# Kernel tuning notes

Hardware: AMD Instinct MI355X
Metric: run time of the kernel (lower is better)

## Reference

```python
import jax, jax.numpy as jnp
import numpy as np

B, P, K, H, W = 32, 8, 17, 192, 192
ALPHA = 0.5
TEMP = 2.0
SIGMA = 3.0


def _bce_with_logits_mean(x, t):
    # numerically stable BCEWithLogitsLoss, reduction='mean'
    return jnp.mean(jnp.maximum(x, 0.0) - x * t + jnp.log1p(jnp.exp(-jnp.abs(x))))


def _kl_batchmean(s_logprob, t_prob):
    # torch KLDivLoss(reduction='batchmean'): sum(t * (log t - log s)) / batch
    return jnp.sum(t_prob * (jnp.log(t_prob) - s_logprob)) / s_logprob.shape[0]


def _keypoints_loss(pred, kps, vis):
    # pred: [B,K,H,W]; kps: [B,P,K,2] normalized; vis: [B,P,K] int
    b, k, h, w = pred.shape
    x = jnp.floor(kps[..., 0] * (w - 1))  # [B,P,K]; coords>=0 so floor == int()
    y = jnp.floor(kps[..., 1] * (h - 1))
    valid = ((vis > 0) & (x >= 0) & (x < w) & (y >= 0) & (y < h)).astype(pred.dtype)
    inv2s2 = 1.0 / (2.0 * SIGMA * SIGMA)
    ax = jnp.arange(w, dtype=pred.dtype)
    ay = jnp.arange(h, dtype=pred.dtype)
    # separable Gaussian: exp(-((a-x)^2+(b-y)^2)/2s^2) = gx(a)*gy(b)
    gx = jnp.exp(-(ax - x[..., None]) ** 2 * inv2s2) * valid[..., None]  # [B,P,K,W]
    gy = jnp.exp(-(ay - y[..., None]) ** 2 * inv2s2)                     # [B,P,K,H]
    # original indexes target[k][a,b] with a over grid_x (W axis); H==W required
    target = jnp.einsum('bpkw,bpkh->bkwh', gx, gy)  # [B,K,W,H] == [B,K,H,W]
    per = jnp.sum((pred - target) ** 2, axis=(1, 2, 3))          # F.mse_loss sum
    denom = jnp.sum(vis, axis=(1, 2)).astype(pred.dtype) + 1e-6
    return jnp.mean(per / denom)


def setup_inputs() -> dict:
    key = jax.random.key(0)
    k1, k2, k3, k4, k5, k6, k7 = jax.random.split(key, 7)
    return {
        's_seg_logits': jax.random.normal(k1, (B, 1, H, W), dtype=jnp.float32),
        's_pose_logits': jax.random.normal(k2, (B, K, H, W), dtype=jnp.float32),
        't_seg_logits': jax.random.normal(k3, (B, 1, H, W), dtype=jnp.float32),
        't_pose_logits': jax.random.normal(k4, (B, K, H, W), dtype=jnp.float32),
        'mask': jax.random.uniform(k5, (B, H, W), dtype=jnp.float32),
        'keypoints': jax.random.uniform(k6, (B, P, K, 2), dtype=jnp.float32),
        'visibilities': jax.random.randint(k7, (B, P, K), 0, 2, dtype=jnp.int32),
    }


def reference(s_seg_logits, s_pose_logits, t_seg_logits, t_pose_logits, mask, keypoints, visibilities):
    # task losses
    task_seg = _bce_with_logits_mean(s_seg_logits, mask[:, None])  # unsqueeze(1)
    task_pose = _keypoints_loss(s_pose_logits, keypoints, visibilities)
    task_loss = task_seg + task_pose
    # segmentation distillation (softmax over channel dim)
    s_seg_lp = jax.nn.log_softmax(s_seg_logits / TEMP, axis=1)
    t_seg_p = jax.nn.softmax(t_seg_logits / TEMP, axis=1)
    seg_distill = _kl_batchmean(s_seg_lp, t_seg_p) * TEMP ** 2
    # pose distillation (softmax over flattened K*H*W)
    s_pose_lp = jax.nn.log_softmax(s_pose_logits.reshape(s_pose_logits.shape[0], -1) / TEMP, axis=1)
    t_pose_p = jax.nn.softmax(t_pose_logits.reshape(t_pose_logits.shape[0], -1) / TEMP, axis=1)
    pose_distill = _kl_batchmean(s_pose_lp, t_pose_p) * TEMP ** 2
    distill_loss = seg_distill + pose_distill
    total = ALPHA * distill_loss + (1.0 - ALPHA) * task_loss
    return total
```

## Files before the change

### kernel.cpp

```cpp
#include <hip/hip_runtime.h>
#include <hip/hip_bf16.h>
#include <math.h>

#define B_   32
#define P_   8
#define K_   17
#define H_   192
#define W_   192
#define HW_  (H_*W_)
#define NROW (K_*HW_)
#define NROW4 (NROW/4)
#define KL_BLK_PER_ROW 153
#define KL_NBLK (B_*KL_BLK_PER_ROW)
#define BCE_NBLK 288
#define KP_SEG 3
#define KP_NBLK (B_*K_*KP_SEG)

__device__ inline float wave_red_sum(float v) {
    for (int o = 32; o; o >>= 1) v += __shfl_xor(v, o, 64);
    return v;
}
__device__ inline float wave_red_max(float v) {
    for (int o = 32; o; o >>= 1) v = fmaxf(v, __shfl_xor(v, o, 64));
    return v;
}
__device__ inline float block_sum(float v, float* sm) {
    v = wave_red_sum(v);
    int w = threadIdx.x >> 6;
    if ((threadIdx.x & 63) == 0) sm[w] = v;
    __syncthreads();
    float r = sm[0] + sm[1] + sm[2] + sm[3];
    __syncthreads();
    return r;
}
__device__ inline float block_max(float v, float* sm) {
    v = wave_red_max(v);
    int w = threadIdx.x >> 6;
    if ((threadIdx.x & 63) == 0) sm[w] = v;
    __syncthreads();
    float r = fmaxf(fmaxf(sm[0], sm[1]), fmaxf(sm[2], sm[3]));
    __syncthreads();
    return r;
}

__global__ void __launch_bounds__(256) bce_kernel(
        const float* __restrict__ x, const float* __restrict__ m,
        float* __restrict__ ws) {
    __shared__ float sm[4];
    const float4* x4 = (const float4*)x;
    const float4* m4 = (const float4*)m;
    int tid = threadIdx.x;
    size_t base = (size_t)blockIdx.x * 1024 + tid;
    float acc = 0.f;
#pragma unroll
    for (int j = 0; j < 4; j++) {
        float4 xv = x4[base + j*256];
        float4 tv = m4[base + j*256];
        acc += fmaxf(xv.x, 0.f) - xv.x*tv.x + log1pf(__expf(-fabsf(xv.x)));
        acc += fmaxf(xv.y, 0.f) - xv.y*tv.y + log1pf(__expf(-fabsf(xv.y)));
        acc += fmaxf(xv.z, 0.f) - xv.z*tv.z + log1pf(__expf(-fabsf(xv.z)));
        acc += fmaxf(xv.w, 0.f) - xv.w*tv.w + log1pf(__expf(-fabsf(xv.w)));
    }
    acc = block_sum(acc, sm);
    if (tid == 0) ws[blockIdx.x] = acc;
}

__global__ void __launch_bounds__(256) kl_kernel(
        const float* __restrict__ s, const float* __restrict__ t,
        float* __restrict__ ws) {
    __shared__ float sm[4];
    int blk = blockIdx.x;
    int b = blk / KL_BLK_PER_ROW;
    int r = blk - b*KL_BLK_PER_ROW;
    size_t base4 = (size_t)b * NROW4 + (size_t)r * 1024;
    const float4* s4 = (const float4*)s + base4;
    const float4* t4 = (const float4*)t + base4;
    int tid = threadIdx.x;

    float u[16], v[16];
#pragma unroll
    for (int j = 0; j < 4; j++) {
        float4 sv = s4[j*256 + tid];
        float4 tv = t4[j*256 + tid];
        v[j*4+0] = sv.x*0.5f; v[j*4+1] = sv.y*0.5f; v[j*4+2] = sv.z*0.5f; v[j*4+3] = sv.w*0.5f;
        u[j*4+0] = tv.x*0.5f; u[j*4+1] = tv.y*0.5f; u[j*4+2] = tv.z*0.5f; u[j*4+3] = tv.w*0.5f;
    }
    float mu = -INFINITY, mv = -INFINITY;
#pragma unroll
    for (int i = 0; i < 16; i++) { mu = fmaxf(mu, u[i]); mv = fmaxf(mv, v[i]); }
    mu = block_max(mu, sm);
    mv = block_max(mv, sm);

    float Zu = 0.f, Zv = 0.f, A = 0.f;
#pragma unroll
    for (int i = 0; i < 16; i++) {
        float e = __expf(u[i] - mu);
        Zu += e;
        A  += e * (u[i] - v[i]);
        Zv += __expf(v[i] - mv);
    }
    Zu = block_sum(Zu, sm);
    Zv = block_sum(Zv, sm);
    A  = block_sum(A,  sm);
    if (tid == 0) {
        float* o = ws + (size_t)blk * 5;
        o[0] = mu; o[1] = Zu; o[2] = mv; o[3] = Zv; o[4] = A;
    }
}

__global__ void __launch_bounds__(256) kp_kernel(
        const float* __restrict__ pred, const float* __restrict__ kps,
        const int* __restrict__ vis, float* __restrict__ ws) {
    __shared__ __align__(16) float gxs[P_][W_];
    __shared__ __align__(16) float gys[P_][H_];
    __shared__ float xk[P_], yk[P_], vld[P_];
    __shared__ float smr[4];

    int blk = blockIdx.x;
    int b   = blk / (K_*KP_SEG);
    int r   = blk - b*(K_*KP_SEG);
    int k   = r / KP_SEG;
    int seg = r - k*KP_SEG;
    int tid = threadIdx.x;

    if (tid < P_) {
        int p = tid;
        float kx = kps[((b*P_ + p)*K_ + k)*2 + 0];
        float ky = kps[((b*P_ + p)*K_ + k)*2 + 1];
        int vv   = vis[(b*P_ + p)*K_ + k];
        float fx = floorf(kx * (float)(W_ - 1));
        float fy = floorf(ky * (float)(H_ - 1));
        bool ok = (vv > 0) && (fx >= 0.f) && (fx < (float)W_) && (fy >= 0.f) && (fy < (float)H_);
        xk[p] = fx; yk[p] = fy; vld[p] = ok ? 1.0f : 0.0f;
    }
    __syncthreads();

    const float inv2s2 = 1.0f / 18.0f;
    for (int e = tid; e < P_*W_; e += 256) {
        int p = e / W_;
        int i = e - p*W_;
        float dx = (float)i - xk[p];
        float dy = (float)i - yk[p];
        gxs[p][i] = __expf(-dx*dx*inv2s2) * vld[p];
        gys[p][i] = __expf(-dy*dy*inv2s2);
    }
    __syncthreads();

    const float* pbase = pred + (size_t)(b*K_ + k) * HW_;
    float acc = 0.f;
#pragma unroll
    for (int it = 0; it < 3; it++) {
        int tau = it*256 + tid;
        int rg = tau / 48;
        int cg = tau - rg*48;
        int i0 = seg*64 + rg*4;
        int j0 = cg*4;
        float4 gx[P_], gy[P_];
#pragma unroll
        for (int p = 0; p < P_; p++) {
            gx[p] = *(const float4*)&gxs[p][i0];
            gy[p] = *(const float4*)&gys[p][j0];
        }
#pragma unroll
        for (int rr = 0; rr < 4; rr++) {
            float4 pv = *(const float4*)(pbase + (i0 + rr)*W_ + j0);
            float t0 = 0.f, t1 = 0.f, t2 = 0.f, t3 = 0.f;
#pragma unroll
            for (int p = 0; p < P_; p++) {
                float g = (rr == 0) ? gx[p].x : (rr == 1) ? gx[p].y : (rr == 2) ? gx[p].z : gx[p].w;
                t0 += g * gy[p].x;
                t1 += g * gy[p].y;
                t2 += g * gy[p].z;
                t3 += g * gy[p].w;
            }
            float d0 = pv.x - t0, d1 = pv.y - t1, d2 = pv.z - t2, d3 = pv.w - t3;
            acc += d0*d0 + d1*d1 + d2*d2 + d3*d3;
        }
    }
    acc = block_sum(acc, smr);
    if (tid == 0) ws[blk] = acc;
}

__global__ void __launch_bounds__(64) finalize_kernel(
        const float* __restrict__ ws_bce, const float* __restrict__ ws_kl,
        const float* __restrict__ ws_kp,  const int* __restrict__ vis,
        float* __restrict__ out) {
    __shared__ float skl[B_], skp[B_];
    int tid = threadIdx.x;

    float bsum = 0.f;
    for (int i = tid; i < BCE_NBLK; i += 64) bsum += ws_bce[i];
    bsum = wave_red_sum(bsum);

    if (tid < B_) {
        int b = tid;
        float Mu = -INFINITY, Zu = 0.f, Mv = -INFINITY, Zv = 0.f, A = 0.f;
        for (int j = 0; j < KL_BLK_PER_ROW; j++) {
            const float* p = ws_kl + (size_t)(b*KL_BLK_PER_ROW + j) * 5;
            float mu = p[0], zu = p[1], mv = p[2], zv = p[3], a = p[4];
            float nm = fmaxf(Mu, mu);
            float e0 = __expf(Mu - nm), e1 = __expf(mu - nm);
            Zu = Zu*e0 + zu*e1;
            A  = A *e0 + a *e1;
            Mu = nm;
            float nm2 = fmaxf(Mv, mv);
            Zv = Zv*__expf(Mv - nm2) + zv*__expf(mv - nm2);
            Mv = nm2;
        }
        float lse_u = Mu + logf(Zu);
        float lse_v = Mv + logf(Zv);
        skl[b] = A / Zu + (lse_v - lse_u);

        float s = 0.f;
        for (int j = 0; j < K_*KP_SEG; j++) s += ws_kp[b*(K_*KP_SEG) + j];
        int d = 0;
        for (int m = 0; m < P_*K_; m++) d += vis[b*(P_*K_) + m];
        skp[b] = s / ((float)d + 1e-6f);
    }
    __syncthreads();

    if (tid == 0) {
        float kl = 0.f, kp = 0.f;
        for (int i = 0; i < B_; i++) { kl += skl[i]; kp += skp[i]; }
        float pose_distill = 4.0f * kl / (float)B_;
        float task_seg  = bsum / (float)(B_ * HW_);
        float task_pose = kp / (float)B_;
        out[0] = 0.5f * pose_distill + 0.5f * (task_seg + task_pose);
    }
}

extern "C" void kernel_launch(void* const* d_in, const int* in_sizes, int n_in,
                              void* d_out, int out_size, void* d_ws, size_t ws_size,
                              hipStream_t stream) {
    const float* s_seg  = (const float*)d_in[0];
    const float* s_pose = (const float*)d_in[1];
    const float* t_pose = (const float*)d_in[3];
    const float* mask   = (const float*)d_in[4];
    const float* kps    = (const float*)d_in[5];
    const int*   vis    = (const int*)d_in[6];
    float* out = (float*)d_out;
    float* ws  = (float*)d_ws;

    float* ws_bce = ws;
    float* ws_kl  = ws + 1024;
    float* ws_kp  = ws + 26624;

    bce_kernel<<<BCE_NBLK, 256, 0, stream>>>(s_seg, mask, ws_bce);
    kl_kernel<<<KL_NBLK, 256, 0, stream>>>(s_pose, t_pose, ws_kl);
    kp_kernel<<<KP_NBLK, 256, 0, stream>>>(s_pose, kps, vis, ws_kp);
    finalize_kernel<<<1, 64, 0, stream>>>(ws_bce, ws_kl, ws_kp, vis, out);
}
```

Before: 240.5 us.

## Fuse KL distillation and BCE into keypoint kernel, drop max-stabilized softmax

Merges the pose KL pass into the keypoint MSE kernel so s_pose is read once and t_pose alongside it. BCE blocks are appended to the same grid, reducing the launches from four to two. The softmax partials no longer subtract a running max, so the finalize step just sums Z and A. This removes the block max reductions and the online rescaling, but it risks overflow for large logits. Finalize is parallelized across 256 threads.

```diff
diff --git a/kernel.cpp b/kernel.cpp
--- a/kernel.cpp
+++ b/kernel.cpp
@@ -8,120 +8,61 @@
 #define H_   192
 #define W_   192
 #define HW_  (H_*W_)
-#define NROW (K_*HW_)
-#define NROW4 (NROW/4)
-#define KL_BLK_PER_ROW 153
-#define KL_NBLK (B_*KL_BLK_PER_ROW)
-#define BCE_NBLK 288
 #define KP_SEG 3
-#define KP_NBLK (B_*K_*KP_SEG)
+#define BLK_PER_B (K_*KP_SEG)
+#define KP_NBLK (B_*BLK_PER_B)
+#define BCE_NBLK 96
+#define TOTAL_BLK (KP_NBLK + BCE_NBLK)
+
+#define WS_KP_OFF  0
+#define WS_KL_OFF  2048
+#define WS_BCE_OFF 8192
 
 __device__ inline float wave_red_sum(float v) {
     for (int o = 32; o; o >>= 1) v += __shfl_xor(v, o, 64);
     return v;
 }
-__device__ inline float wave_red_max(float v) {
-    for (int o = 32; o; o >>= 1) v = fmaxf(v, __shfl_xor(v, o, 64));
-    return v;
-}
-__device__ inline float block_sum(float v, float* sm) {
-    v = wave_red_sum(v);
-    int w = threadIdx.x >> 6;
-    if ((threadIdx.x & 63) == 0) sm[w] = v;
-    __syncthreads();
-    float r = sm[0] + sm[1] + sm[2] + sm[3];
-    __syncthreads();
-    return r;
-}
-__device__ inline float block_max(float v, float* sm) {
-    v = wave_red_max(v);
-    int w = threadIdx.x >> 6;
-    if ((threadIdx.x & 63) == 0) sm[w] = v;
-    __syncthreads();
-    float r = fmaxf(fmaxf(sm[0], sm[1]), fmaxf(sm[2], sm[3]));
-    __syncthreads();
-    return r;
-}
-
-__global__ void __launch_bounds__(256) bce_kernel(
-        const float* __restrict__ x, const float* __restrict__ m,
+
+__global__ void __launch_bounds__(256) main_kernel(
+        const float* __restrict__ s_pose, const float* __restrict__ t_pose,
+        const float* __restrict__ kps,    const int* __restrict__ vis,
+        const float* __restrict__ s_seg,  const float* __restrict__ mask,
         float* __restrict__ ws) {
-    __shared__ float sm[4];
-    const float4* x4 = (const float4*)x;
-    const float4* m4 = (const float4*)m;
-    int tid = threadIdx.x;
-    size_t base = (size_t)blockIdx.x * 1024 + tid;
-    float acc = 0.f;
-#pragma unroll
-    for (int j = 0; j < 4; j++) {
-        float4 xv = x4[base + j*256];
-        float4 tv = m4[base + j*256];
-        acc += fmaxf(xv.x, 0.f) - xv.x*tv.x + log1pf(__expf(-fabsf(xv.x)));
-        acc += fmaxf(xv.y, 0.f) - xv.y*tv.y + log1pf(__expf(-fabsf(xv.y)));
-        acc += fmaxf(xv.z, 0.f) - xv.z*tv.z + log1pf(__expf(-fabsf(xv.z)));
-        acc += fmaxf(xv.w, 0.f) - xv.w*tv.w + log1pf(__expf(-fabsf(xv.w)));
-    }
-    acc = block_sum(acc, sm);
-    if (tid == 0) ws[blockIdx.x] = acc;
-}
-
-__global__ void __launch_bounds__(256) kl_kernel(
-        const float* __restrict__ s, const float* __restrict__ t,
-        float* __restrict__ ws) {
-    __shared__ float sm[4];
-    int blk = blockIdx.x;
-    int b = blk / KL_BLK_PER_ROW;
-    int r = blk - b*KL_BLK_PER_ROW;
-    size_t base4 = (size_t)b * NROW4 + (size_t)r * 1024;
-    const float4* s4 = (const float4*)s + base4;
-    const float4* t4 = (const float4*)t + base4;
-    int tid = threadIdx.x;
-
-    float u[16], v[16];
-#pragma unroll
-    for (int j = 0; j < 4; j++) {
-        float4 sv = s4[j*256 + tid];
-        float4 tv = t4[j*256 + tid];
-        v[j*4+0] = sv.x*0.5f; v[j*4+1] = sv.y*0.5f; v[j*4+2] = sv.z*0.5f; v[j*4+3] = sv.w*0.5f;
-        u[j*4+0] = tv.x*0.5f; u[j*4+1] = tv.y*0.5f; u[j*4+2] = tv.z*0.5f; u[j*4+3] = tv.w*0.5f;
-    }
-    float mu = -INFINITY, mv = -INFINITY;
-#pragma unroll
-    for (int i = 0; i < 16; i++) { mu = fmaxf(mu, u[i]); mv = fmaxf(mv, v[i]); }
-    mu = block_max(mu, sm);
-    mv = block_max(mv, sm);
-
-    float Zu = 0.f, Zv = 0.f, A = 0.f;
-#pragma unroll
-    for (int i = 0; i < 16; i++) {
-        float e = __expf(u[i] - mu);
-        Zu += e;
-        A  += e * (u[i] - v[i]);
-        Zv += __expf(v[i] - mv);
-    }
-    Zu = block_sum(Zu, sm);
-    Zv = block_sum(Zv, sm);
-    A  = block_sum(A,  sm);
-    if (tid == 0) {
-        float* o = ws + (size_t)blk * 5;
-        o[0] = mu; o[1] = Zu; o[2] = mv; o[3] = Zv; o[4] = A;
-    }
-}
-
-__global__ void __launch_bounds__(256) kp_kernel(
-        const float* __restrict__ pred, const float* __restrict__ kps,
-        const int* __restrict__ vis, float* __restrict__ ws) {
     __shared__ __align__(16) float gxs[P_][W_];
     __shared__ __align__(16) float gys[P_][H_];
     __shared__ float xk[P_], yk[P_], vld[P_];
-    __shared__ float smr[4];
+    __shared__ float red[4][4];
 
     int blk = blockIdx.x;
-    int b   = blk / (K_*KP_SEG);
-    int r   = blk - b*(K_*KP_SEG);
+    int tid = threadIdx.x;
+
+    if (blk >= KP_NBLK) {
+        int bidx = blk - KP_NBLK;
+        const float4* x4 = (const float4*)s_seg;
+        const float4* m4 = (const float4*)mask;
+        size_t base = (size_t)bidx * 3072 + tid;
+        float acc = 0.f;
+#pragma unroll
+        for (int j = 0; j < 12; j++) {
+            float4 xv = x4[base + j*256];
+            float4 tv = m4[base + j*256];
+            acc += fmaxf(xv.x, 0.f) - xv.x*tv.x + log1pf(__expf(-fabsf(xv.x)));
+            acc += fmaxf(xv.y, 0.f) - xv.y*tv.y + log1pf(__expf(-fabsf(xv.y)));
+            acc += fmaxf(xv.z, 0.f) - xv.z*tv.z + log1pf(__expf(-fabsf(xv.z)));
+            acc += fmaxf(xv.w, 0.f) - xv.w*tv.w + log1pf(__expf(-fabsf(xv.w)));
+        }
+        acc = wave_red_sum(acc);
+        if ((tid & 63) == 0) red[0][tid >> 6] = acc;
+        __syncthreads();
+        if (tid == 0)
+            ws[WS_BCE_OFF + bidx] = red[0][0] + red[0][1] + red[0][2] + red[0][3];
+        return;
+    }
+
+    int b   = blk / BLK_PER_B;
+    int r   = blk - b*BLK_PER_B;
     int k   = r / KP_SEG;
     int seg = r - k*KP_SEG;
-    int tid = threadIdx.x;
 
     if (tid < P_) {
         int p = tid;
@@ -146,8 +87,11 @@
     }
     __syncthreads();
 
-    const float* pbase = pred + (size_t)(b*K_ + k) * HW_;
-    float acc = 0.f;
+    const size_t off = (size_t)(b*K_ + k) * HW_;
+    const float* pbase = s_pose + off;
+    const float* tbase = t_pose + off;
+
+    float mse = 0.f, Zu = 0.f, Zv = 0.f, A = 0.f;
 #pragma unroll
     for (int it = 0; it < 3; it++) {
         int tau = it*256 + tid;
@@ -163,7 +107,10 @@
         }
 #pragma unroll
         for (int rr = 0; rr < 4; rr++) {
-            float4 pv = *(const float4*)(pbase + (i0 + rr)*W_ + j0);
+            const float* rowp = pbase + (i0 + rr)*W_ + j0;
+            const float* rowt = tbase + (i0 + rr)*W_ + j0;
+            float4 pv = *(const float4*)rowp;
+            float4 tv = *(const float4*)rowt;
             float t0 = 0.f, t1 = 0.f, t2 = 0.f, t3 = 0.f;
 #pragma unroll
             for (int p = 0; p < P_; p++) {
@@ -174,57 +121,83 @@
                 t3 += g * gy[p].w;
             }
             float d0 = pv.x - t0, d1 = pv.y - t1, d2 = pv.z - t2, d3 = pv.w - t3;
-            acc += d0*d0 + d1*d1 + d2*d2 + d3*d3;
-        }
-    }
-    acc = block_sum(acc, smr);
-    if (tid == 0) ws[blk] = acc;
-}
-
-__global__ void __launch_bounds__(64) finalize_kernel(
-        const float* __restrict__ ws_bce, const float* __restrict__ ws_kl,
-        const float* __restrict__ ws_kp,  const int* __restrict__ vis,
+            mse += d0*d0 + d1*d1 + d2*d2 + d3*d3;
+            {
+                float u, v, eu;
+                u = tv.x*0.5f; v = pv.x*0.5f; eu = __expf(u); Zu += eu; A += eu*(u - v); Zv += __expf(v);
+                u = tv.y*0.5f; v = pv.y*0.5f; eu = __expf(u); Zu += eu; A += eu*(u - v); Zv += __expf(v);
+                u = tv.z*0.5f; v = pv.z*0.5f; eu = __expf(u); Zu += eu; A += eu*(u - v); Zv += __expf(v);
+                u = tv.w*0.5f; v = pv.w*0.5f; eu = __expf(u); Zu += eu; A += eu*(u - v); Zv += __expf(v);
+            }
+        }
+    }
+
+    mse = wave_red_sum(mse);
+    Zu  = wave_red_sum(Zu);
+    Zv  = wave_red_sum(Zv);
+    A   = wave_red_sum(A);
+    int w = tid >> 6;
+    if ((tid & 63) == 0) {
+        red[w][0] = mse; red[w][1] = Zu; red[w][2] = Zv; red[w][3] = A;
+    }
+    __syncthreads();
+    if (tid == 0) {
+        float m = 0.f, zu = 0.f, zv = 0.f, a = 0.f;
+#pragma unroll
+        for (int q = 0; q < 4; q++) {
+            m += red[q][0]; zu += red[q][1]; zv += red[q][2]; a += red[q][3];
+        }
+        ws[WS_KP_OFF + blk] = m;
+        float* o = ws + WS_KL_OFF + (size_t)blk * 3;
+        o[0] = zu; o[1] = zv; o[2] = a;
+    }
+}
+
+__global__ void __launch_bounds__(256) finalize_kernel(
+        const float* __restrict__ ws, const int* __restrict__ vis,
         float* __restrict__ out) {
+    __shared__ float rkp[B_][8], rzu[B_][8], rzv[B_][8], ra[B_][8];
+    __shared__ int   rvs[B_][8];
     __shared__ float skl[B_], skp[B_];
+    __shared__ float bw[4];
     int tid = threadIdx.x;
-
-    float bsum = 0.f;
-    for (int i = tid; i < BCE_NBLK; i += 64) bsum += ws_bce[i];
-    bsum = wave_red_sum(bsum);
+    int b = tid >> 3, s = tid & 7;
+
+    float kp = 0.f, zu = 0.f, zv = 0.f, a = 0.f;
+    for (int j = s; j < BLK_PER_B; j += 8) {
+        int blk = b*BLK_PER_B + j;
+        kp += ws[WS_KP_OFF + blk];
+        const float* p = ws + WS_KL_OFF + (size_t)blk * 3;
+        zu += p[0]; zv += p[1]; a += p[2];
+    }
+    int vs = 0;
+    for (int m = s; m < P_*K_; m += 8) vs += vis[b*(P_*K_) + m];
+    rkp[b][s] = kp; rzu[b][s] = zu; rzv[b][s] = zv; ra[b][s] = a; rvs[b][s] = vs;
+
+    float bce = (tid < BCE_NBLK) ? ws[WS_BCE_OFF + tid] : 0.f;
+    bce = wave_red_sum(bce);
+    if ((tid & 63) == 0) bw[tid >> 6] = bce;
+    __syncthreads();
 
     if (tid < B_) {
-        int b = tid;
-        float Mu = -INFINITY, Zu = 0.f, Mv = -INFINITY, Zv = 0.f, A = 0.f;
-        for (int j = 0; j < KL_BLK_PER_ROW; j++) {
-            const float* p = ws_kl + (size_t)(b*KL_BLK_PER_ROW + j) * 5;
-            float mu = p[0], zu = p[1], mv = p[2], zv = p[3], a = p[4];
-            float nm = fmaxf(Mu, mu);
-            float e0 = __expf(Mu - nm), e1 = __expf(mu - nm);
-            Zu = Zu*e0 + zu*e1;
-            A  = A *e0 + a *e1;
-            Mu = nm;
-            float nm2 = fmaxf(Mv, mv);
-            Zv = Zv*__expf(Mv - nm2) + zv*__expf(mv - nm2);
-            Mv = nm2;
-        }
-        float lse_u = Mu + logf(Zu);
-        float lse_v = Mv + logf(Zv);
-        skl[b] = A / Zu + (lse_v - lse_u);
-
-        float s = 0.f;
-        for (int j = 0; j < K_*KP_SEG; j++) s += ws_kp[b*(K_*KP_SEG) + j];
-        int d = 0;
-        for (int m = 0; m < P_*K_; m++) d += vis[b*(P_*K_) + m];
-        skp[b] = s / ((float)d + 1e-6f);
+        float KP = 0.f, ZU = 0.f, ZV = 0.f, AA = 0.f; int VS = 0;
+#pragma unroll
+        for (int q = 0; q < 8; q++) {
+            KP += rkp[tid][q]; ZU += rzu[tid][q]; ZV += rzv[tid][q];
+            AA += ra[tid][q];  VS += rvs[tid][q];
+        }
+        skl[tid] = AA/ZU + (logf(ZV) - logf(ZU));
+        skp[tid] = KP / ((float)VS + 1e-6f);
     }
     __syncthreads();
 
     if (tid == 0) {
-        float kl = 0.f, kp = 0.f;
-        for (int i = 0; i < B_; i++) { kl += skl[i]; kp += skp[i]; }
+        float kl = 0.f, kpv = 0.f;
+        for (int i = 0; i < B_; i++) { kl += skl[i]; kpv += skp[i]; }
+        float bsum = bw[0] + bw[1] + bw[2] + bw[3];
         float pose_distill = 4.0f * kl / (float)B_;
         float task_seg  = bsum / (float)(B_ * HW_);
-        float task_pose = kp / (float)B_;
+        float task_pose = kpv / (float)B_;
         out[0] = 0.5f * pose_distill + 0.5f * (task_seg + task_pose);
     }
 }
@@ -241,12 +214,7 @@
     float* out = (float*)d_out;
     float* ws  = (float*)d_ws;
 
-    float* ws_bce = ws;
-    float* ws_kl  = ws + 1024;
-    float* ws_kp  = ws + 26624;
-
-    bce_kernel<<<BCE_NBLK, 256, 0, stream>>>(s_seg, mask, ws_bce);
-    kl_kernel<<<KL_NBLK, 256, 0, stream>>>(s_pose, t_pose, ws_kl);
-    kp_kernel<<<KP_NBLK, 256, 0, stream>>>(s_pose, kps, vis, ws_kp);
-    finalize_kernel<<<1, 64, 0, stream>>>(ws_bce, ws_kl, ws_kp, vis, out);
-}
+    main_kernel<<<TOTAL_BLK, 256, 0, stream>>>(s_pose, t_pose, kps, vis,
+                                               s_seg, mask, ws);
+    finalize_kernel<<<1, 256, 0, stream>>>(ws, vis, out);
+}
```

Result: faster. 208.4 us (-13.3%).
